# Kernel tuning notes

Hardware: AMD Instinct MI355X
Metric: run time of the kernel (lower is better)

The kernel has to match this reference:

```python
import jax, jax.numpy as jnp
import numpy as np

B, N, M, DIM = 64, 512, 512, 64
GAMMA = 1.0
BANDWIDTH = 0.0  # 0 => Sakoe-Chiba pruning disabled (bandwidth=None in torch module)
BIG = 1e10       # finite stand-in for +inf boundary; exp(-BIG/gamma) underflows to 0


def setup_inputs() -> dict:
    key = jax.random.key(0)
    kx, ky, kl = jax.random.split(key, 3)
    X = jax.random.normal(kx, (B, N, DIM), dtype=jnp.float32)
    Y = jax.random.normal(ky, (B, M, DIM), dtype=jnp.float32)
    # valid lengths in [N//2, N]
    lengths_x = jax.random.randint(kl, (B,), N // 2, N + 1, dtype=jnp.int32)
    return {"X": X, "Y": Y, "lengths_x": lengths_x}


def _pairwise_sq_dist(x, y):
    # D[b,i,j] = sum_d (x[b,i,d] - y[b,j,d])^2, via the gemm expansion to
    # avoid materializing a [B,N,M,D] tensor.
    x2 = jnp.sum(x * x, axis=-1)[:, :, None]            # [B,N,1]
    y2 = jnp.sum(y * y, axis=-1)[:, None, :]            # [B,1,M]
    xy = jnp.einsum("bnd,bmd->bnm", x, y)               # [B,N,M]
    return x2 + y2 - 2.0 * xy


def _softdtw(D, lengths):
    # Anti-diagonal wavefront DP. Diagonal k holds R[i, k-i] (1-based DP grid,
    # R[0,0]=0, all other boundary cells = BIG (stand-in for +inf)).
    Bb, Nn, Mm = D.shape
    ivec = jnp.arange(Nn + 1)                            # storage index i = 0..N
    rows = jnp.clip(ivec - 1, 0, Nn - 1)                 # D row index (static)
    len_mask = ivec[None, :] <= lengths[:, None]         # rows i>L stay at inf

    d_km2 = jnp.full((Bb, Nn + 1), BIG, D.dtype).at[:, 0].set(0.0)  # diag k=0
    d_km1 = jnp.full((Bb, Nn + 1), BIG, D.dtype)                     # diag k=1

    def step(carry, k):
        d2, d1 = carry
        j = k - ivec                                     # (N+1,)
        cols = jnp.clip(j - 1, 0, Mm - 1)
        Dk = D[:, rows, cols]                            # D[b, i-1, j-1] -> (B, N+1)
        # neighbors: d2[i-1]=R[i-1,j-1], d1[i-1]=R[i-1,j], d1[i]=R[i,j-1]
        r0 = -jnp.roll(d2, 1, axis=1) / GAMMA
        r1 = -jnp.roll(d1, 1, axis=1) / GAMMA
        r2 = -d1 / GAMMA
        softmin = -GAMMA * jax.nn.logsumexp(jnp.stack([r0, r1, r2]), axis=0)
        valid = (ivec >= 1) & (j >= 1) & (j <= Mm)
        if BANDWIDTH > 0:
            valid = valid & (jnp.abs(ivec - j) <= BANDWIDTH)
        valid = valid[None, :] & len_mask
        new = jnp.where(valid, Dk + softmin, BIG)
        return (d1, new), new

    ks = jnp.arange(2, Nn + Mm + 1)
    _, diags = jax.lax.scan(step, (d_km2, d_km1), ks)    # (N+M-1, B, N+1)
    # R[b, L_b, M] lives on diagonal k = L_b + M (scan index k-2) at position i=L_b
    return diags[lengths + Mm - 2, jnp.arange(Bb), lengths]


def reference(X, Y, lengths_x):
    D = _pairwise_sq_dist(X, Y)
    return _softdtw(D, lengths_x)
```

## Files before the change

kernel.cpp:

```cpp
#include <hip/hip_runtime.h>

constexpr int Bc   = 64;
constexpr int Nc   = 512;
constexpr int Mc   = 512;
constexpr int DIMc = 64;
constexpr float BIGc = 1e10f;
constexpr int CELLS = Nc * Mc;
constexpr float LOG2E = 1.442695041f;
constexpr float LN2   = 0.6931471806f;

constexpr int STRIDE   = 65;
constexpr int SBUF     = 32 * STRIDE;
constexpr int WAVE_LDS = 2 * SBUF;
constexpr int RING_OFF = 8 * WAVE_LDS;
constexpr int LDS_WORDS = RING_OFF + 8 * 64;

struct TrueC  { static constexpr bool value = true;  };
struct FalseC { static constexpr bool value = false; };

__device__ __forceinline__ float dpp_shr1_f(float v, float old) {
    return __builtin_bit_cast(float, __builtin_amdgcn_update_dpp(
        __builtin_bit_cast(int, old), __builtin_bit_cast(int, v), 0x138, 0xF, 0xF, false));
}
__device__ __forceinline__ float f4c(const float4 v, int c) {
    switch (c & 3) { case 0: return v.x; case 1: return v.y;
                     case 2: return v.z; default: return v.w; }
}
__device__ __forceinline__ void f4set(float4& d, int c, float v) {
    switch (c & 3) { case 0: d.x = v; break; case 1: d.y = v; break;
                     case 2: d.z = v; break; default: d.w = v; }
}

__global__ __launch_bounds__(256)
void compute_D(const float* __restrict__ X, const float* __restrict__ Y,
               float* __restrict__ Dc)
{
    const int b   = blockIdx.x;
    const int nt  = blockIdx.y;
    const int tid = threadIdx.x;
    const int ty  = tid >> 4, tx = tid & 15;

    __shared__ float Xs[DIMc][68];
    __shared__ float Ys[DIMc][68];

    const float* Xb = X + ((size_t)b * Nc + (size_t)nt * 64) * DIMc;
    const float* Yb = Y + (size_t)b * Mc * DIMc;
    float*       Db = Dc + (size_t)b * CELLS;
    const int n0 = nt * 64;

    {
        const float4* Xb4 = reinterpret_cast<const float4*>(Xb);
        for (int c4 = tid; c4 < 64 * DIMc / 4; c4 += 256) {
            float4 v = Xb4[c4];
            const int n = c4 >> 4, k0 = (c4 & 15) * 4;
            Xs[k0+0][n] = v.x; Xs[k0+1][n] = v.y; Xs[k0+2][n] = v.z; Xs[k0+3][n] = v.w;
        }
    }

    for (int mt = 0; mt < Mc / 64; ++mt) {
        __syncthreads();
        {
            const float4* Yb4 = reinterpret_cast<const float4*>(Yb + (size_t)mt * 64 * DIMc);
            for (int c4 = tid; c4 < 64 * DIMc / 4; c4 += 256) {
                float4 v = Yb4[c4];
                const int n = c4 >> 4, k0 = (c4 & 15) * 4;
                Ys[k0+0][n] = v.x; Ys[k0+1][n] = v.y; Ys[k0+2][n] = v.z; Ys[k0+3][n] = v.w;
            }
        }
        __syncthreads();

        float acc[4][4];
        #pragma unroll
        for (int r = 0; r < 4; ++r)
            #pragma unroll
            for (int cc = 0; cc < 4; ++cc) acc[r][cc] = 0.f;

        #pragma unroll 8
        for (int k = 0; k < DIMc; ++k) {
            float4 xv = *reinterpret_cast<const float4*>(&Xs[k][ty * 4]);
            float4 yv = *reinterpret_cast<const float4*>(&Ys[k][tx * 4]);
            float xr[4] = {xv.x, xv.y, xv.z, xv.w};
            float yr[4] = {yv.x, yv.y, yv.z, yv.w};
            #pragma unroll
            for (int r = 0; r < 4; ++r)
                #pragma unroll
                for (int cc = 0; cc < 4; ++cc) {
                    float d = xr[r] - yr[cc];
                    acc[r][cc] = fmaf(d, d, acc[r][cc]);
                }
        }

        #pragma unroll
        for (int r = 0; r < 4; ++r) {
            const int n = n0 + ty * 4 + r;
            float4 st = make_float4(acc[r][0]*LOG2E, acc[r][1]*LOG2E,
                                    acc[r][2]*LOG2E, acc[r][3]*LOG2E);
            *reinterpret_cast<float4*>(&Db[(size_t)n * Mc + mt * 64 + tx * 4]) = st;
        }
    }
}

__global__ __launch_bounds__(512)
void softdtw_sys8(const float* __restrict__ Dc, const int* __restrict__ lengths,
                  float* __restrict__ out)
{
    extern __shared__ float lds[];
    const int b    = blockIdx.x;
    const int t    = threadIdx.x;
    const int lane = t & 63;
    const int W    = __builtin_amdgcn_readfirstlane(t >> 6);
    const int L    = lengths[b];
    const int r    = (W << 6) + lane;
    const int i    = r + 1;
    const float* Dbat = Dc + (size_t)b * CELLS;

    float* stageW = lds + W * WAVE_LDS;

    if (t < 64) lds[RING_OFF + t] = BIGc;
    __syncthreads();

    const bool l0   = (lane == 0);
    const bool iok  = (i <= L);
    const int  gcap = (i == L) ? (L + 510) : -1;
    const int  qlL  = (L + 510) >> 5;
    const bool rowsOK = ((W << 6) + 64) <= L;
    const int  q0 = 2 * W;
    const int  ql = min(2 * W + 17, qlL);
    const int  cmax = 8 + qlL;

    float own = BIGc, nb1 = BIGc, nb2 = BIGc, res = 0.f;
    if (W == 0 && l0) nb2 = 0.f;

    const int lbase = (((W << 6) + (lane >> 3)) * 511) + ((lane & 7) << 2);
    const int wbw   = ((lane & 7) << 2) * STRIDE + (lane >> 3);

    auto stageLoad = [&](int qn, float4* sreg) {
        const int gb = qn * 32;
        #pragma unroll
        for (int u = 0; u < 8; ++u) {
            const int idx = lbase + u * (8 * 511) + gb;
            if (idx <= CELLS - 4) {
                sreg[u] = *reinterpret_cast<const float4*>(Dbat + idx);
            } else {
                sreg[u] = make_float4(Dbat[CELLS-3], Dbat[CELLS-2], Dbat[CELLS-1], 0.f);
            }
        }
    };
    auto stageWrite = [&](int qn, const float4* sreg) {
        float* wb = stageW + (qn & 1) * SBUF + wbw;
        #pragma unroll
        for (int u = 0; u < 8; ++u) {
            wb[0 * STRIDE + u * 8] = sreg[u].x;
            wb[1 * STRIDE + u * 8] = sreg[u].y;
            wb[2 * STRIDE + u * 8] = sreg[u].z;
            wb[3 * STRIDE + u * 8] = sreg[u].w;
        }
    };

    {
        float4 s0[8];
        stageLoad(q0, s0);
        stageWrite(q0, s0);
    }

    for (int c = 0; c < cmax; ++c) {
        const int q = c - W;
        if (q >= q0 && q <= ql) {
            const int g0 = q * 32;

            float4 rv[8];
            {
                const float4* rp = reinterpret_cast<const float4*>(
                    lds + RING_OFF + W * 64 + (g0 & 63));
                #pragma unroll
                for (int u = 0; u < 8; ++u) rv[u] = rp[u];
            }

            const bool doNext = (q + 1 <= ql);
            float4 sreg[8];
            if (doNext) stageLoad(q + 1, sreg);

            const float* rb = stageW + (q & 1) * SBUF + lane;
            float Dwin[32];
            #pragma unroll
            for (int s = 0; s < 32; ++s) Dwin[s] = rb[s * STRIDE];

            float4 expv[8];
            const bool fastC = rowsOK && q >= q0 + 2 && q <= q0 + 15 && q != qlL;

            auto body = [&](auto FASTC) {
                constexpr bool FAST = decltype(FASTC)::value;
                #pragma unroll
                for (int s = 0; s < 32; ++s) {
                    const int g = g0 + s;
                    const float mn = fminf(nb2, fminf(nb1, own));
                    const float e  = __builtin_amdgcn_exp2f(mn - nb2)
                                   + __builtin_amdgcn_exp2f(mn - nb1)
                                   + __builtin_amdgcn_exp2f(mn - own);
                    const float sm = mn - __builtin_amdgcn_logf(e);
                    float v = Dwin[s] + sm;
                    if (!FAST) {
                        const bool jok = (unsigned)(g - r) < (unsigned)Mc;
                        v = (jok && iok) ? v : BIGc;
                        res = (g == gcap) ? v : res;
                    }
                    f4set(expv[s >> 2], s, v);
                    const float sh = dpp_shr1_f(v, BIGc);
                    nb2 = nb1;
                    nb1 = l0 ? f4c(rv[s >> 2], s) : sh;
                    own = v;
                }
            };
            if (fastC) body(TrueC{}); else body(FalseC{});

            if (doNext) stageWrite(q + 1, sreg);

            if (W < 7 && lane == 63) {
                float* re = lds + RING_OFF + (W + 1) * 64 + (g0 & 63);
                #pragma unroll
                for (int u = 0; u < 8; ++u)
                    reinterpret_cast<float4*>(re)[u] = expv[u];
            }
        } else if (W > 0 && q == q0 - 1) {
            const float p1 = lds[RING_OFF + W * 64 + 63];
            const float p0 = lds[RING_OFF + W * 64 + 62];
            nb1 = l0 ? p1 : nb1;
            nb2 = l0 ? p0 : nb2;
        }
        asm volatile("s_waitcnt lgkmcnt(0)" ::: "memory");
        __builtin_amdgcn_s_barrier();
        asm volatile("" ::: "memory");
    }

    if (i == L) out[b] = res * LN2;
}

__global__ __launch_bounds__(512)
void softdtw_fused(const float* __restrict__ X, const float* __restrict__ Y,
                   const int* __restrict__ lengths, float* __restrict__ out)
{
    const int b = blockIdx.x;
    const int t = threadIdx.x;
    const int i = t + 1;
    const int L = lengths[b];

    __shared__ float diag[3][Nc + 1];
    for (int c = t; c <= Nc; c += 512) {
        diag[0][c] = (c == 0) ? 0.f : BIGc;
        diag[1][c] = BIGc;
    }
    float xr[DIMc];
    const float* Xrow = X + ((size_t)b * Nc + t) * DIMc;
    #pragma unroll
    for (int d = 0; d < DIMc; d += 4) {
        float4 v = *reinterpret_cast<const float4*>(Xrow + d);
        xr[d] = v.x; xr[d+1] = v.y; xr[d+2] = v.z; xr[d+3] = v.w;
    }
    const float* Yb = Y + (size_t)b * Mc * DIMc;
    __syncthreads();

    float result = BIGc;
    int cur = 2, p1 = 1, p2 = 0;
    for (int k = 2; k <= Nc + Mc; ++k) {
        const int j = k - i;
        const bool valid = (j >= 1) && (j <= Mc) && (i <= L);
        float Dval = 0.f;
        if (valid) {
            const float* Yrow = Yb + (size_t)(j - 1) * DIMc;
            float s = 0.f;
            #pragma unroll
            for (int d = 0; d < DIMc; d += 4) {
                float4 v = *reinterpret_cast<const float4*>(Yrow + d);
                float d0 = xr[d] - v.x, d1 = xr[d+1] - v.y;
                float d2 = xr[d+2] - v.z, d3 = xr[d+3] - v.w;
                s = fmaf(d0,d0,s); s = fmaf(d1,d1,s); s = fmaf(d2,d2,s); s = fmaf(d3,d3,s);
            }
            Dval = s;
        }
        const float a2 = diag[p2][i-1], a1 = diag[p1][i-1], a0 = diag[p1][i];
        const float mn = fminf(a2, fminf(a1, a0));
        const float sm = mn - __logf(__expf(mn-a2) + __expf(mn-a1) + __expf(mn-a0));
        const float val = valid ? (Dval + sm) : BIGc;
        diag[cur][i] = val;
        if (t == 0) diag[cur][0] = BIGc;
        if (k == L + Mc && i == L) result = val;
        __syncthreads();
        const int tmp = p2; p2 = p1; p1 = cur; cur = tmp;
    }
    if (i == L) out[b] = result;
}

extern "C" void kernel_launch(void* const* d_in, const int* in_sizes, int n_in,
                              void* d_out, int out_size, void* d_ws, size_t ws_size,
                              hipStream_t stream) {
    const float* X = (const float*)d_in[0];
    const float* Y = (const float*)d_in[1];
    const int* lengths = (const int*)d_in[2];
    float* out = (float*)d_out;

    const size_t need = (size_t)Bc * CELLS * sizeof(float);
    if (ws_size >= need) {
        float* Dc = (float*)d_ws;
        compute_D<<<dim3(Bc, Nc / 64), 256, 0, stream>>>(X, Y, Dc);
        softdtw_sys8<<<Bc, 512, LDS_WORDS * 4, stream>>>(Dc, lengths, out);
    } else {
        softdtw_fused<<<Bc, 512, 0, stream>>>(X, Y, lengths, out);
    }
}
```

Baseline: 219.8 us.

## Store D in anti-diagonal layout and stream DP inputs directly from global

The distance kernel now uses 128x128 tiles and transposes each tile through LDS so that D is written in anti-diagonal-major order. The DP kernel then reads each diagonal contiguously, one coalesced load per step straight into registers, which removes the per-wave LDS staging buffers and the transpose from the critical wavefront loop. In exchange the distance kernel issues scattered, partly uncoalesced diagonal writes and needs about 100KB of LDS per block. The DP loop now depends on global-load latency being hidden within each step.

```diff
diff --git a/kernel.cpp b/kernel.cpp
--- a/kernel.cpp
+++ b/kernel.cpp
@@ -9,14 +9,22 @@
 constexpr float LOG2E = 1.442695041f;
 constexpr float LN2   = 0.6931471806f;
 
-constexpr int STRIDE   = 65;
-constexpr int SBUF     = 32 * STRIDE;
-constexpr int WAVE_LDS = 2 * SBUF;
-constexpr int RING_OFF = 8 * WAVE_LDS;
-constexpr int LDS_WORDS = RING_OFF + 8 * 64;
-
 struct TrueC  { static constexpr bool value = true;  };
 struct FalseC { static constexpr bool value = false; };
+
+__device__ __forceinline__ int diag_off(int g) {
+    if (g < Mc) return g * (g + 1) / 2;
+    int e = g - Mc;
+    return Mc * (Mc + 1) / 2 + e * (Nc - 1) - e * (e - 1) / 2;
+}
+__device__ __forceinline__ int diag_nmin(int g) {
+    return (g > Mc - 1) ? (g - (Mc - 1)) : 0;
+}
+__device__ __forceinline__ int dOffm(int g) {
+    if (g < 512) return g * (g + 1) / 2;
+    int e = g - 512;
+    return 131328 + e * 511 - e * (e - 1) / 2 - (g - 511);
+}
 
 __device__ __forceinline__ float dpp_shr1_f(float v, float old) {
     return __builtin_bit_cast(float, __builtin_amdgcn_update_dpp(
@@ -31,71 +39,100 @@
                      case 2: d.z = v; break; default: d.w = v; }
 }
 
+constexpr int XS_OFF = 0;
+constexpr int YS_OFF = 64 * 132;
+constexpr int CT_OFF = 2 * 64 * 132;
+constexpr int A_LDS_WORDS = CT_OFF + 128 * 130;
+
 __global__ __launch_bounds__(256)
-void compute_D(const float* __restrict__ X, const float* __restrict__ Y,
-               float* __restrict__ Dc)
+void compute_D_diag(const float* __restrict__ X, const float* __restrict__ Y,
+                    float* __restrict__ Dc)
 {
+    extern __shared__ float lds[];
+    float* Xs = lds + XS_OFF;
+    float* Ys = lds + YS_OFF;
+    float* Ct = lds + CT_OFF;
+
     const int b   = blockIdx.x;
     const int nt  = blockIdx.y;
     const int tid = threadIdx.x;
     const int ty  = tid >> 4, tx = tid & 15;
 
-    __shared__ float Xs[DIMc][68];
-    __shared__ float Ys[DIMc][68];
-
-    const float* Xb = X + ((size_t)b * Nc + (size_t)nt * 64) * DIMc;
+    const float* Xb = X + ((size_t)b * Nc + (size_t)nt * 128) * DIMc;
     const float* Yb = Y + (size_t)b * Mc * DIMc;
     float*       Db = Dc + (size_t)b * CELLS;
-    const int n0 = nt * 64;
+    const int n0 = nt * 128;
 
     {
         const float4* Xb4 = reinterpret_cast<const float4*>(Xb);
-        for (int c4 = tid; c4 < 64 * DIMc / 4; c4 += 256) {
+        for (int c4 = tid; c4 < 128 * DIMc / 4; c4 += 256) {
             float4 v = Xb4[c4];
             const int n = c4 >> 4, k0 = (c4 & 15) * 4;
-            Xs[k0+0][n] = v.x; Xs[k0+1][n] = v.y; Xs[k0+2][n] = v.z; Xs[k0+3][n] = v.w;
-        }
-    }
-
-    for (int mt = 0; mt < Mc / 64; ++mt) {
+            Xs[(k0+0)*132 + n] = v.x; Xs[(k0+1)*132 + n] = v.y;
+            Xs[(k0+2)*132 + n] = v.z; Xs[(k0+3)*132 + n] = v.w;
+        }
+    }
+
+    for (int mt = 0; mt < 4; ++mt) {
         __syncthreads();
         {
-            const float4* Yb4 = reinterpret_cast<const float4*>(Yb + (size_t)mt * 64 * DIMc);
-            for (int c4 = tid; c4 < 64 * DIMc / 4; c4 += 256) {
+            const float4* Yb4 = reinterpret_cast<const float4*>(Yb + (size_t)mt * 128 * DIMc);
+            for (int c4 = tid; c4 < 128 * DIMc / 4; c4 += 256) {
                 float4 v = Yb4[c4];
-                const int n = c4 >> 4, k0 = (c4 & 15) * 4;
-                Ys[k0+0][n] = v.x; Ys[k0+1][n] = v.y; Ys[k0+2][n] = v.z; Ys[k0+3][n] = v.w;
+                const int m = c4 >> 4, k0 = (c4 & 15) * 4;
+                Ys[(k0+0)*132 + m] = v.x; Ys[(k0+1)*132 + m] = v.y;
+                Ys[(k0+2)*132 + m] = v.z; Ys[(k0+3)*132 + m] = v.w;
             }
         }
         __syncthreads();
 
-        float acc[4][4];
+        float acc[8][8];
         #pragma unroll
-        for (int r = 0; r < 4; ++r)
+        for (int r = 0; r < 8; ++r)
             #pragma unroll
-            for (int cc = 0; cc < 4; ++cc) acc[r][cc] = 0.f;
-
-        #pragma unroll 8
+            for (int cc = 0; cc < 8; ++cc) acc[r][cc] = 0.f;
+
+        #pragma unroll 2
         for (int k = 0; k < DIMc; ++k) {
-            float4 xv = *reinterpret_cast<const float4*>(&Xs[k][ty * 4]);
-            float4 yv = *reinterpret_cast<const float4*>(&Ys[k][tx * 4]);
-            float xr[4] = {xv.x, xv.y, xv.z, xv.w};
-            float yr[4] = {yv.x, yv.y, yv.z, yv.w};
+            float4 xa = *reinterpret_cast<const float4*>(&Xs[k*132 + ty*8]);
+            float4 xb = *reinterpret_cast<const float4*>(&Xs[k*132 + ty*8 + 4]);
+            float4 ya = *reinterpret_cast<const float4*>(&Ys[k*132 + tx*8]);
+            float4 yb = *reinterpret_cast<const float4*>(&Ys[k*132 + tx*8 + 4]);
+            float xr[8] = {xa.x,xa.y,xa.z,xa.w, xb.x,xb.y,xb.z,xb.w};
+            float yr[8] = {ya.x,ya.y,ya.z,ya.w, yb.x,yb.y,yb.z,yb.w};
             #pragma unroll
-            for (int r = 0; r < 4; ++r)
+            for (int r = 0; r < 8; ++r)
                 #pragma unroll
-                for (int cc = 0; cc < 4; ++cc) {
+                for (int cc = 0; cc < 8; ++cc) {
                     float d = xr[r] - yr[cc];
                     acc[r][cc] = fmaf(d, d, acc[r][cc]);
                 }
         }
 
         #pragma unroll
-        for (int r = 0; r < 4; ++r) {
-            const int n = n0 + ty * 4 + r;
-            float4 st = make_float4(acc[r][0]*LOG2E, acc[r][1]*LOG2E,
+        for (int r = 0; r < 8; ++r) {
+            float4 s0 = make_float4(acc[r][0]*LOG2E, acc[r][1]*LOG2E,
                                     acc[r][2]*LOG2E, acc[r][3]*LOG2E);
-            *reinterpret_cast<float4*>(&Db[(size_t)n * Mc + mt * 64 + tx * 4]) = st;
+            float4 s1 = make_float4(acc[r][4]*LOG2E, acc[r][5]*LOG2E,
+                                    acc[r][6]*LOG2E, acc[r][7]*LOG2E);
+            *reinterpret_cast<float4*>(&Ct[(ty*8+r)*130 + tx*8])     = s0;
+            *reinterpret_cast<float4*>(&Ct[(ty*8+r)*130 + tx*8 + 4]) = s1;
+        }
+        __syncthreads();
+
+        const int grp  = tid >> 6;
+        const int lane = tid & 63;
+        const int g00  = n0 + mt * 128;
+        for (int d = grp; d < 255; d += 4) {
+            const int tn_lo = max(0, d - 127);
+            const int tn_hi = min(127, d);
+            const int len   = tn_hi - tn_lo + 1;
+            const int dg    = g00 + d;
+            const int base  = diag_off(dg) - diag_nmin(dg) + n0;
+            for (int o = lane; o < len; o += 64) {
+                const int tn = tn_lo + o;
+                Db[base + tn] = Ct[tn*130 + (d - tn)];
+            }
         }
     }
 }
@@ -104,7 +141,7 @@
 void softdtw_sys8(const float* __restrict__ Dc, const int* __restrict__ lengths,
                   float* __restrict__ out)
 {
-    extern __shared__ float lds[];
+    __shared__ float ring[8][64];
     const int b    = blockIdx.x;
     const int t    = threadIdx.x;
     const int lane = t & 63;
@@ -114,9 +151,7 @@
     const int i    = r + 1;
     const float* Dbat = Dc + (size_t)b * CELLS;
 
-    float* stageW = lds + W * WAVE_LDS;
-
-    if (t < 64) lds[RING_OFF + t] = BIGc;
+    if (t < 64) ring[0][t] = BIGc;
     __syncthreads();
 
     const bool l0   = (lane == 0);
@@ -131,36 +166,17 @@
     float own = BIGc, nb1 = BIGc, nb2 = BIGc, res = 0.f;
     if (W == 0 && l0) nb2 = 0.f;
 
-    const int lbase = (((W << 6) + (lane >> 3)) * 511) + ((lane & 7) << 2);
-    const int wbw   = ((lane & 7) << 2) * STRIDE + (lane >> 3);
-
-    auto stageLoad = [&](int qn, float4* sreg) {
-        const int gb = qn * 32;
+    float Dwin[32];
+    {
+        int sb = dOffm(q0 * 32);
+        int gg = q0 * 32;
         #pragma unroll
-        for (int u = 0; u < 8; ++u) {
-            const int idx = lbase + u * (8 * 511) + gb;
-            if (idx <= CELLS - 4) {
-                sreg[u] = *reinterpret_cast<const float4*>(Dbat + idx);
-            } else {
-                sreg[u] = make_float4(Dbat[CELLS-3], Dbat[CELLS-2], Dbat[CELLS-1], 0.f);
-            }
-        }
-    };
-    auto stageWrite = [&](int qn, const float4* sreg) {
-        float* wb = stageW + (qn & 1) * SBUF + wbw;
-        #pragma unroll
-        for (int u = 0; u < 8; ++u) {
-            wb[0 * STRIDE + u * 8] = sreg[u].x;
-            wb[1 * STRIDE + u * 8] = sreg[u].y;
-            wb[2 * STRIDE + u * 8] = sreg[u].z;
-            wb[3 * STRIDE + u * 8] = sreg[u].w;
-        }
-    };
-
-    {
-        float4 s0[8];
-        stageLoad(q0, s0);
-        stageWrite(q0, s0);
+        for (int s = 0; s < 32; ++s) {
+            Dwin[s] = Dbat[sb + r];
+            int d1 = (gg < 512) ? (gg + 1) : (1023 - gg);
+            sb += d1 - ((gg >= 511) ? 1 : 0);
+            ++gg;
+        }
     }
 
     for (int c = 0; c < cmax; ++c) {
@@ -170,20 +186,14 @@
 
             float4 rv[8];
             {
-                const float4* rp = reinterpret_cast<const float4*>(
-                    lds + RING_OFF + W * 64 + (g0 & 63));
+                const float4* rp = reinterpret_cast<const float4*>(&ring[W][g0 & 63]);
                 #pragma unroll
                 for (int u = 0; u < 8; ++u) rv[u] = rp[u];
             }
 
             const bool doNext = (q + 1 <= ql);
-            float4 sreg[8];
-            if (doNext) stageLoad(q + 1, sreg);
-
-            const float* rb = stageW + (q & 1) * SBUF + lane;
-            float Dwin[32];
-            #pragma unroll
-            for (int s = 0; s < 32; ++s) Dwin[s] = rb[s * STRIDE];
+            int gN  = doNext ? (g0 + 32) : 0;
+            int sbN = dOffm(gN);
 
             float4 expv[8];
             const bool fastC = rowsOK && q >= q0 + 2 && q <= q0 + 15 && q != qlL;
@@ -204,6 +214,12 @@
                         v = (jok && iok) ? v : BIGc;
                         res = (g == gcap) ? v : res;
                     }
+                    Dwin[s] = Dbat[sbN + r];
+                    {
+                        int d1 = (gN < 512) ? (gN + 1) : (1023 - gN);
+                        sbN += d1 - ((gN >= 511) ? 1 : 0);
+                        ++gN;
+                    }
                     f4set(expv[s >> 2], s, v);
                     const float sh = dpp_shr1_f(v, BIGc);
                     nb2 = nb1;
@@ -213,17 +229,15 @@
             };
             if (fastC) body(TrueC{}); else body(FalseC{});
 
-            if (doNext) stageWrite(q + 1, sreg);
-
             if (W < 7 && lane == 63) {
-                float* re = lds + RING_OFF + (W + 1) * 64 + (g0 & 63);
+                float* re = &ring[W + 1][g0 & 63];
                 #pragma unroll
                 for (int u = 0; u < 8; ++u)
                     reinterpret_cast<float4*>(re)[u] = expv[u];
             }
         } else if (W > 0 && q == q0 - 1) {
-            const float p1 = lds[RING_OFF + W * 64 + 63];
-            const float p0 = lds[RING_OFF + W * 64 + 62];
+            const float p1 = ring[W][63];
+            const float p0 = ring[W][62];
             nb1 = l0 ? p1 : nb1;
             nb2 = l0 ? p0 : nb2;
         }
@@ -301,8 +315,8 @@
     const size_t need = (size_t)Bc * CELLS * sizeof(float);
     if (ws_size >= need) {
         float* Dc = (float*)d_ws;
-        compute_D<<<dim3(Bc, Nc / 64), 256, 0, stream>>>(X, Y, Dc);
-        softdtw_sys8<<<Bc, 512, LDS_WORDS * 4, stream>>>(Dc, lengths, out);
+        compute_D_diag<<<dim3(Bc, 4), 256, A_LDS_WORDS * 4, stream>>>(X, Y, Dc);
+        softdtw_sys8<<<Bc, 512, 0, stream>>>(Dc, lengths, out);
     } else {
         softdtw_fused<<<Bc, 512, 0, stream>>>(X, Y, lengths, out);
     }
```

Measured after the change: 252.0 us. +14.6%, slower.
